# Kernel tuning notes

Hardware: AMD Instinct MI355X
Metric: run time of the kernel (lower is better)

The kernel has to match this reference:

```python
import jax, jax.numpy as jnp
import numpy as np

NEG_INF = -9e15  # mask value used by the original module
LEAKY_SLOPE = 0.2


def setup_inputs() -> dict:
    key = jax.random.key(0)
    k1, k2, k3, k4 = jax.random.split(key, 4)
    B, N, F_in = 4, 2048, 128
    H, head_dim = 4, 32
    h = jax.random.normal(k1, (B, N, F_in), dtype=jnp.float32)
    adj = jax.random.randint(k2, (N, N), 0, 2, dtype=jnp.int32)
    W = jax.random.normal(k3, (H, F_in, head_dim), dtype=jnp.float32)
    a = jax.random.normal(k4, (H, 2 * head_dim, 1), dtype=jnp.float32)
    return {"h": h, "adj": adj, "W": W, "a": a}


def reference(h, adj, W, a):
    # h: (B, N, F_in); adj: (N, N) int; W: (H, F_in, D); a: (H, 2D, 1)
    D = W.shape[-1]
    Wh = jnp.einsum('bnf,hfd->bhnd', h, W)          # (B, H, N, D)
    # Original builds [Wh_i || Wh_j] @ a. Split a so that
    # e_ij = Wh_i . a_src + Wh_j . a_dst  (identical math, no N^2*2D concat).
    a_src = a[:, :D, 0]                              # (H, D)
    a_dst = a[:, D:, 0]                              # (H, D)
    e_src = jnp.einsum('bhnd,hd->bhn', Wh, a_src)    # (B, H, N)
    e_dst = jnp.einsum('bhnd,hd->bhn', Wh, a_dst)    # (B, H, N)
    e = jax.nn.leaky_relu(e_src[..., :, None] + e_dst[..., None, :],
                          negative_slope=LEAKY_SLOPE)  # (B, H, N, N)
    masked = jnp.where(adj[None, None] > 0, e, NEG_INF)
    attn = jax.nn.softmax(masked, axis=-1)           # dropout: eval mode (identity)
    out = jnp.einsum('bhij,bhjd->bhid', attn, Wh)    # (B, H, N, D)
    B, H, N, _ = out.shape
    # concat heads along feature dim == transpose to (B, N, H, D) then merge
    return out.transpose(0, 2, 1, 3).reshape(B, N, H * D)
```

## Files before the change

kernel.cpp:

```cpp
#include <hip/hip_runtime.h>
#include <hip/hip_bf16.h>

typedef unsigned short u16;
using f32x4 = __attribute__((ext_vector_type(4))) float;
using short8 = __attribute__((ext_vector_type(8))) short;

constexpr int B_ = 4, N_ = 2048, FIN = 128, H_ = 4, D_ = 32;
constexpr int BH = B_ * H_;
constexpr float LOG2E = 1.4426950408889634f;

static __device__ __forceinline__ float bitsel(int m, float a, unsigned int bu) {
  return __uint_as_float((__float_as_uint(a) & (unsigned)m) | (bu & ~(unsigned)m));
}

constexpr int NPB = 16;

__global__ __launch_bounds__(256) void wh_kernel(
    const float* __restrict__ h, const float* __restrict__ W,
    const float* __restrict__ a, u16* __restrict__ WhT,
    float* __restrict__ es, float* __restrict__ ed) {
  __shared__ float hsh[NPB][FIN];
  __shared__ float part[NPB][H_][D_];
  const int t = threadIdx.x;
  const int fh = t >> 7, hh = (t >> 5) & 3, d = t & 31;

  float Wr[64];
#pragma unroll
  for (int ff = 0; ff < 64; ++ff)
    Wr[ff] = W[hh * (FIN * D_) + (fh * 64 + ff) * D_ + d];

  const int n0 = blockIdx.x * NPB;
  for (int idx = t; idx < NPB * FIN; idx += 256)
    hsh[idx >> 7][idx & 127] = h[(size_t)n0 * FIN + idx];
  __syncthreads();

  float accs[NPB];
#pragma unroll
  for (int r = 0; r < NPB; ++r) {
    float acc = 0.f;
    const float* hr = &hsh[r][fh * 64];
#pragma unroll
    for (int f4 = 0; f4 < 16; ++f4) {
      float4 hv = *(const float4*)(hr + f4 * 4);
      acc += hv.x * Wr[f4 * 4 + 0];
      acc += hv.y * Wr[f4 * 4 + 1];
      acc += hv.z * Wr[f4 * 4 + 2];
      acc += hv.w * Wr[f4 * 4 + 3];
    }
    accs[r] = acc;
  }
  if (fh == 0) {
#pragma unroll
    for (int r = 0; r < NPB; ++r) part[r][hh][d] = accs[r];
  }
  __syncthreads();
  if (fh == 1) {
    const int b = n0 / N_;
    const int bh = b * H_ + hh;
    const int n0r = n0 & (N_ - 1);
    const float asrc = a[hh * 2 * D_ + d];
    const float adst = a[hh * 2 * D_ + D_ + d];
    union { u16 s[16]; uint4 q[2]; } wbuf;
#pragma unroll
    for (int r = 0; r < NPB; ++r) {
      const float wh = accs[r] + part[r][hh][d];
      union { __hip_bfloat16 h; u16 u; } cv;
      cv.h = __float2bfloat16(wh);
      wbuf.s[r] = cv.u;
      float vs = wh * asrc, vd = wh * adst;
#pragma unroll
      for (int o = 16; o >= 1; o >>= 1) {
        vs += __shfl_xor(vs, o, 64);
        vd += __shfl_xor(vd, o, 64);
      }
      if (d == 0) {
        es[(size_t)bh * N_ + n0r + r] = vs * LOG2E;
        ed[(size_t)bh * N_ + n0r + r] = vd * LOG2E;
      }
    }
    u16* dst = WhT + ((size_t)(bh * 32 + d)) * N_ + n0r;
    *(uint4*)dst = wbuf.q[0];
    *(uint4*)(dst + 8) = wbuf.q[1];
  }
}

__global__ __launch_bounds__(256) void pack_kernel(
    const int* __restrict__ adj, unsigned long long* __restrict__ mask) {
  const int gid = blockIdx.x * 256 + threadIdx.x;
  const int wdx = gid >> 6;
  const int lane = threadIdx.x & 63;
  const int i = wdx >> 5;
  const int jb = (wdx & 31) << 6;
  const int v = adj[(size_t)i * N_ + jb + lane];
  const unsigned long long m = __ballot(v > 0);
  if (lane == 0) mask[wdx] = m;
}

constexpr int ROWS = 16;
constexpr int NSTEP = 16;

__global__ __launch_bounds__(256, 8) void attn_kernel(
    const float* __restrict__ es, const float* __restrict__ ed,
    const u16* __restrict__ WhT, const unsigned int* __restrict__ mask32,
    float* __restrict__ out) {
  __shared__ __align__(16) char arena[12352];
  __shared__ float essh[ROWS], rmsh[ROWS];
  __shared__ float sumsh[4][16];

  float* edsh = (float*)arena;
  unsigned int* maskw = (unsigned int*)(arena + 8192);

  const int bh = blockIdx.x >> 7;
  const int i0 = (blockIdx.x & 127) * ROWS;
  const int tid = threadIdx.x, lane = tid & 63, w = tid >> 6;
  const int jq = w;

  const float* edb = ed + (size_t)bh * N_;
  *(float4*)&edsh[tid * 8] = *(const float4*)(edb + tid * 8);
  *(float4*)&edsh[tid * 8 + 4] = *(const float4*)(edb + tid * 8 + 4);
  const unsigned int* mrow = mask32 + (size_t)i0 * 64;
#pragma unroll
  for (int q = 0; q < 4; ++q) {
    const int idx = tid + q * 256;
    maskw[(idx >> 6) * 65 + (idx & 63)] = mrow[(idx >> 6) * 64 + (idx & 63)];
  }
  if (tid < ROWS) essh[tid] = es[(size_t)bh * N_ + i0 + tid];
  __syncthreads();

  {
    const unsigned int NEGU = __float_as_uint(-3.0e38f);
    float mx0 = -3.0e38f, mx1 = -3.0e38f, mx2 = -3.0e38f, mx3 = -3.0e38f;
    const int l31 = lane & 31, lh = lane >> 5;
#pragma unroll 8
    for (int q = 0; q < 32; ++q) {
      const float edv = edsh[q * 64 + lane];
      const int base = w * 4 * 65 + q * 2 + lh;
      const int b0 = __builtin_amdgcn_sbfe((int)maskw[base], l31, 1);
      const int b1 = __builtin_amdgcn_sbfe((int)maskw[base + 65], l31, 1);
      const int b2 = __builtin_amdgcn_sbfe((int)maskw[base + 130], l31, 1);
      const int b3 = __builtin_amdgcn_sbfe((int)maskw[base + 195], l31, 1);
      mx0 = fmaxf(mx0, bitsel(b0, edv, NEGU));
      mx1 = fmaxf(mx1, bitsel(b1, edv, NEGU));
      mx2 = fmaxf(mx2, bitsel(b2, edv, NEGU));
      mx3 = fmaxf(mx3, bitsel(b3, edv, NEGU));
    }
#pragma unroll
    for (int o = 32; o >= 1; o >>= 1) {
      mx0 = fmaxf(mx0, __shfl_xor(mx0, o, 64));
      mx1 = fmaxf(mx1, __shfl_xor(mx1, o, 64));
      mx2 = fmaxf(mx2, __shfl_xor(mx2, o, 64));
      mx3 = fmaxf(mx3, __shfl_xor(mx3, o, 64));
    }
    if (lane == 0) {
      rmsh[w * 4 + 0] = mx0;
      rmsh[w * 4 + 1] = mx1;
      rmsh[w * 4 + 2] = mx2;
      rmsh[w * 4 + 3] = mx3;
    }
  }
  __syncthreads();

  const int row16 = lane & 15, kg = lane >> 4;
  const float esr = essh[row16];
  const float xm = esr + rmsh[row16];
  const float mxr = fmaxf(xm, 0.2f * xm);
  const float cpos = esr - mxr;
  const float cneg = 0.2f * esr - mxr;
  const unsigned int NEGZ = __float_as_uint(-1.0e30f);

  const u16* wb0 = WhT + ((size_t)(bh * 32 + row16)) * N_ + jq * 512 + kg * 8;
  const u16* wb1 = wb0 + (size_t)16 * N_;
  const unsigned int* mwp = maskw + row16 * 65 + jq * 16;
  const float* edq = edsh + jq * 512 + kg * 8;
  const int kg8 = kg << 3;

  short8 ones;
#pragma unroll
  for (int q = 0; q < 8; ++q) ones[q] = (short)0x3F80;

  f32x4 c0 = {}, c1 = {}, csum = {};

#pragma unroll 4
  for (int s = 0; s < NSTEP; ++s) {
    const short8 b0 = *(const short8*)(wb0 + s * 32);
    const short8 b1 = *(const short8*)(wb1 + s * 32);

    const unsigned int mw = mwp[s] >> kg8;
    const float4 ea = *(const float4*)(edq + s * 32);
    const float4 eb = *(const float4*)(edq + s * 32 + 4);
    const float ev[8] = {ea.x, ea.y, ea.z, ea.w, eb.x, eb.y, eb.z, eb.w};
    float p[8];
#pragma unroll
    for (int j = 0; j < 8; ++j) {
      const float edv = ev[j];
      const float zp = edv + cpos;
      const float zn = __builtin_fmaf(edv, 0.2f, cneg);
      const float z = fmaxf(zp, zn);
      const int mbit = __builtin_amdgcn_sbfe((int)mw, j, 1);
      p[j] = __builtin_amdgcn_exp2f(bitsel(mbit, z, NEGZ));
    }
    union { unsigned int u[4]; short8 v8; } af;
    asm("v_cvt_pk_bf16_f32 %0, %1, %2" : "=v"(af.u[0]) : "v"(p[0]), "v"(p[1]));
    asm("v_cvt_pk_bf16_f32 %0, %1, %2" : "=v"(af.u[1]) : "v"(p[2]), "v"(p[3]));
    asm("v_cvt_pk_bf16_f32 %0, %1, %2" : "=v"(af.u[2]) : "v"(p[4]), "v"(p[5]));
    asm("v_cvt_pk_bf16_f32 %0, %1, %2" : "=v"(af.u[3]) : "v"(p[6]), "v"(p[7]));

    c0 = __builtin_amdgcn_mfma_f32_16x16x32_bf16(af.v8, b0, c0, 0, 0, 0);
    c1 = __builtin_amdgcn_mfma_f32_16x16x32_bf16(af.v8, b1, c1, 0, 0, 0);
    csum = __builtin_amdgcn_mfma_f32_16x16x32_bf16(af.v8, ones, csum, 0, 0, 0);
  }

  __syncthreads();

  float* redc = (float*)arena;
#pragma unroll
  for (int r = 0; r < 4; ++r) {
    redc[(jq * 16 + kg * 4 + r) * 33 + row16] = c0[r];
    redc[(jq * 16 + kg * 4 + r) * 33 + 16 + row16] = c1[r];
  }
  if (row16 == 0) {
#pragma unroll
    for (int r = 0; r < 4; ++r) sumsh[jq][kg * 4 + r] = csum[r];
  }
  __syncthreads();

  if (tid < 128) {
    const int r = tid >> 3;
    const int c4 = (tid & 7) * 4;
    const float inv =
        1.f / fmaxf(sumsh[0][r] + sumsh[1][r] + sumsh[2][r] + sumsh[3][r],
                    1e-30f);
    float4 o;
    const float* p0 = &redc[(0 * 16 + r) * 33 + c4];
    const float* p1 = &redc[(1 * 16 + r) * 33 + c4];
    const float* p2 = &redc[(2 * 16 + r) * 33 + c4];
    const float* p3 = &redc[(3 * 16 + r) * 33 + c4];
    o.x = (p0[0] + p1[0] + p2[0] + p3[0]) * inv;
    o.y = (p0[1] + p1[1] + p2[1] + p3[1]) * inv;
    o.z = (p0[2] + p1[2] + p2[2] + p3[2]) * inv;
    o.w = (p0[3] + p1[3] + p2[3] + p3[3]) * inv;
    const int b = bh >> 2, hh = bh & 3;
    *(float4*)&out[((size_t)(b * N_ + i0 + r)) * (H_ * D_) + hh * 32 + c4] = o;
  }
}

extern "C" void kernel_launch(void* const* d_in, const int* in_sizes, int n_in,
                              void* d_out, int out_size, void* d_ws,
                              size_t ws_size, hipStream_t stream) {
  const float* h = (const float*)d_in[0];
  const int* adj = (const int*)d_in[1];
  const float* W = (const float*)d_in[2];
  const float* a = (const float*)d_in[3];
  char* ws = (char*)d_ws;
  u16* WhT = (u16*)ws;
  float* es = (float*)(ws + (2u << 20));
  float* ed = (float*)(ws + (2u << 20) + (128u << 10));
  unsigned long long* mask =
      (unsigned long long*)(ws + (2u << 20) + (256u << 10));
  float* out = (float*)d_out;

  wh_kernel<<<B_ * N_ / NPB, 256, 0, stream>>>(h, W, a, WhT, es, ed);
  pack_kernel<<<N_ * N_ / 256, 256, 0, stream>>>(adj, mask);
  attn_kernel<<<BH * (N_ / ROWS), 256, 0, stream>>>(
      es, ed, WhT, (const unsigned int*)mask, out);
}
```

Baseline: 125.5 us.

## Prefetch WhT tiles, preload mask words, and coarsen pack kernel per wave

Measured after the change: 124.8 us. Within noise of the previous version (-0.5%).

```diff
diff --git a/kernel.cpp b/kernel.cpp
--- a/kernel.cpp
+++ b/kernel.cpp
@@ -84,16 +84,21 @@
   }
 }
 
+constexpr int PACKW = N_ * N_ / 64;
+
 __global__ __launch_bounds__(256) void pack_kernel(
     const int* __restrict__ adj, unsigned long long* __restrict__ mask) {
-  const int gid = blockIdx.x * 256 + threadIdx.x;
-  const int wdx = gid >> 6;
+  const int wave = (blockIdx.x * 256 + threadIdx.x) >> 6;
   const int lane = threadIdx.x & 63;
-  const int i = wdx >> 5;
-  const int jb = (wdx & 31) << 6;
-  const int v = adj[(size_t)i * N_ + jb + lane];
-  const unsigned long long m = __ballot(v > 0);
-  if (lane == 0) mask[wdx] = m;
+#pragma unroll
+  for (int t = 0; t < 8; ++t) {
+    const int wdx = wave * 8 + t;
+    const int i = wdx >> 5;
+    const int jb = (wdx & 31) << 6;
+    const int v = adj[(size_t)i * N_ + jb + lane];
+    const unsigned long long m = __ballot(v > 0);
+    if (lane == 0) mask[wdx] = m;
+  }
 }
 
 constexpr int ROWS = 16;
@@ -166,26 +171,32 @@
   const float mxr = fmaxf(xm, 0.2f * xm);
   const float cpos = esr - mxr;
   const float cneg = 0.2f * esr - mxr;
-  const unsigned int NEGZ = __float_as_uint(-1.0e30f);
+
+  const unsigned int* mwp = maskw + row16 * 65 + jq * 16;
+  const int kg8 = kg << 3;
+  unsigned int mreg[16];
+#pragma unroll
+  for (int s = 0; s < NSTEP; ++s) mreg[s] = mwp[s] >> kg8;
 
   const u16* wb0 = WhT + ((size_t)(bh * 32 + row16)) * N_ + jq * 512 + kg * 8;
   const u16* wb1 = wb0 + (size_t)16 * N_;
-  const unsigned int* mwp = maskw + row16 * 65 + jq * 16;
   const float* edq = edsh + jq * 512 + kg * 8;
-  const int kg8 = kg << 3;
 
   short8 ones;
 #pragma unroll
   for (int q = 0; q < 8; ++q) ones[q] = (short)0x3F80;
 
   f32x4 c0 = {}, c1 = {}, csum = {};
-
-#pragma unroll 4
+  short8 b0 = *(const short8*)wb0;
+  short8 b1 = *(const short8*)wb1;
+
+#pragma unroll
   for (int s = 0; s < NSTEP; ++s) {
-    const short8 b0 = *(const short8*)(wb0 + s * 32);
-    const short8 b1 = *(const short8*)(wb1 + s * 32);
-
-    const unsigned int mw = mwp[s] >> kg8;
+    const int sn = (s + 1 < NSTEP) ? (s + 1) : s;
+    const short8 nb0 = *(const short8*)(wb0 + sn * 32);
+    const short8 nb1 = *(const short8*)(wb1 + sn * 32);
+
+    const unsigned int mw = mreg[s];
     const float4 ea = *(const float4*)(edq + s * 32);
     const float4 eb = *(const float4*)(edq + s * 32 + 4);
     const float ev[8] = {ea.x, ea.y, ea.z, ea.w, eb.x, eb.y, eb.z, eb.w};
@@ -196,8 +207,9 @@
       const float zp = edv + cpos;
       const float zn = __builtin_fmaf(edv, 0.2f, cneg);
       const float z = fmaxf(zp, zn);
+      const float e = __builtin_amdgcn_exp2f(z);
       const int mbit = __builtin_amdgcn_sbfe((int)mw, j, 1);
-      p[j] = __builtin_amdgcn_exp2f(bitsel(mbit, z, NEGZ));
+      p[j] = bitsel(mbit, e, 0u);
     }
     union { unsigned int u[4]; short8 v8; } af;
     asm("v_cvt_pk_bf16_f32 %0, %1, %2" : "=v"(af.u[0]) : "v"(p[0]), "v"(p[1]));
@@ -208,6 +220,8 @@
     c0 = __builtin_amdgcn_mfma_f32_16x16x32_bf16(af.v8, b0, c0, 0, 0, 0);
     c1 = __builtin_amdgcn_mfma_f32_16x16x32_bf16(af.v8, b1, c1, 0, 0, 0);
     csum = __builtin_amdgcn_mfma_f32_16x16x32_bf16(af.v8, ones, csum, 0, 0, 0);
+    b0 = nb0;
+    b1 = nb1;
   }
 
   __syncthreads();
@@ -260,7 +274,7 @@
   float* out = (float*)d_out;
 
   wh_kernel<<<B_ * N_ / NPB, 256, 0, stream>>>(h, W, a, WhT, es, ed);
-  pack_kernel<<<N_ * N_ / 256, 256, 0, stream>>>(adj, mask);
+  pack_kernel<<<PACKW / (8 * 4), 256, 0, stream>>>(adj, mask);
   attn_kernel<<<BH * (N_ / ROWS), 256, 0, stream>>>(
       es, ed, WhT, (const unsigned int*)mask, out);
 }
```
